# Kernel tuning notes

Hardware: AMD Instinct MI355X
Metric: run time of the kernel (lower is better)

Reference implementation:

```python
import jax, jax.numpy as jnp
import numpy as np
from jax import lax

R = 0.7          # ball-query radius
K = 32           # max neighbors per ball
STRIDE = 32      # spatial stride -> M = N // STRIDE anchors
COUT = 1024      # mlp_planes[0]


def fps(pts, M):
    """Furthest point sampling. pts: [N,3] -> int32 [M] indices (starts at 0, like CUDA FPS)."""
    N = pts.shape[0]

    def step(carry, _):
        d2, last = carry
        dist = jnp.sum((pts - pts[last]) ** 2, axis=-1)
        d2 = jnp.minimum(d2, dist)
        return (d2, jnp.argmax(d2).astype(jnp.int32)), last

    init = (jnp.full((N,), 1e10, dtype=pts.dtype), jnp.int32(0))
    _, idxs = lax.scan(step, init, None, length=M)
    return idxs


def ball_query(neigh, anchor):
    """neigh: [N,3], anchor: [M,3] -> int32 [M,K]: first K in-radius neighbor indices,
    padded with the first valid index (matching pointnet2 ball_query semantics)."""
    N = neigh.shape[0]
    d2 = jnp.sum((anchor[:, None, :] - neigh[None, :, :]) ** 2, axis=-1)  # [M,N]
    key = jnp.where(d2 < R * R, jnp.arange(N), N)  # valid points keep their position
    order = jnp.argsort(key, axis=-1)[:, :K]       # stable: first-in-order valid indices
    valid = jnp.take_along_axis(key, order, axis=-1) < N
    return jnp.where(valid, order, order[:, :1])


def setup_inputs() -> dict:
    key = jax.random.key(0)
    k1, k2 = jax.random.split(key)
    xyzs = jax.random.uniform(k1, (4, 16, 2048, 3), dtype=jnp.float32)  # points in unit cube
    w_d = jax.random.normal(k2, (COUT, 4), dtype=jnp.float32) * 0.1     # conv_d 1x1 weight
    return {"xyzs": xyzs, "w_d": w_d}


def reference(xyzs, w_d):
    B, T, N, _ = xyzs.shape
    M = N // STRIDE
    # replicate temporal padding [1,1]
    pad = jnp.concatenate([xyzs[:, :1], xyzs, xyzs[:, -1:]], axis=1)  # [B,T+2,N,3]

    anchors_src = pad[:, 1:-1].reshape(B * T, N, 3)
    aidx = jax.vmap(lambda p: fps(p, M))(anchors_src)                         # [BT,M]
    anchor = jnp.take_along_axis(anchors_src, aidx[..., None], axis=1)        # [BT,M,3]

    feat = None
    for dt in (-1, 0, 1):  # temporal kernel taps
        neigh = pad[:, 1 + dt: 1 + dt + T].reshape(B * T, N, 3)
        idx = jax.vmap(ball_query)(neigh, anchor)                             # [BT,M,K]
        grouped = jnp.take_along_axis(
            neigh, idx.reshape(B * T, M * K)[..., None], axis=1
        ).reshape(B * T, M, K, 3)
        disp = grouped - anchor[:, :, None, :]                                # xyz displacement
        d4 = jnp.concatenate(
            [disp, jnp.full((B * T, M, K, 1), float(dt), disp.dtype)], axis=-1
        )                                                                     # [BT,M,K,4]
        f = jax.nn.relu(jnp.einsum('nmkc,oc->nmko', d4, w_d))                 # 1x1 conv + ReLU
        f = jnp.max(f, axis=2)                                                # spatial max pool -> [BT,M,C]
        feat = f if feat is None else feat + f                                # temporal sum pool

    new_xyzs = anchor.reshape(B, T, M, 3)
    new_features = feat.reshape(B, T, M, COUT).transpose(0, 1, 3, 2)          # [B,T,C,M]
    return new_xyzs, new_features
```

## Files before the change

kernel.cpp:

```cpp
#include <hip/hip_runtime.h>
#include <hip/hip_fp16.h>

#define NB 4
#define NT 16
#define NN 2048
#define NM 64
#define NK 32
#define NC 1024

static __device__ inline __half2 h2max(__half2 a, __half2 b) {
    unsigned int ai = *(unsigned int*)&a, bi = *(unsigned int*)&b, di;
    asm("v_pk_max_f16 %0, %1, %2" : "=v"(di) : "v"(ai), "v"(bi));
    return *(__half2*)&di;
}
static __device__ inline unsigned long long u64max(unsigned long long a, unsigned long long b) {
    return a > b ? a : b;
}

__global__ __launch_bounds__(256) void fps_kernel(const float* __restrict__ xyzs,
                                                  float* __restrict__ out_xyz) {
    const int bt = blockIdx.x;
    const float* pts = xyzs + (size_t)bt * NN * 3;
    __shared__ float sX[NN], sY[NN], sZ[NN];
    __shared__ unsigned long long sPart[2][4];
    __shared__ float sAnchor[NM * 3];
    const int tid = threadIdx.x;
    const int lane = tid & 63, wave = tid >> 6;
    float px[8], py[8], pz[8], d2[8];
    #pragma unroll
    for (int j = 0; j < 8; ++j) {
        const int p = tid + 256 * j;
        px[j] = pts[p * 3 + 0];
        py[j] = pts[p * 3 + 1];
        pz[j] = pts[p * 3 + 2];
        sX[p] = px[j]; sY[p] = py[j]; sZ[p] = pz[j];
        d2[j] = 1e10f;
    }
    __syncthreads();
    int last = 0;
    for (int it = 0; it < NM; ++it) {
        const float lx = sX[last], ly = sY[last], lz = sZ[last];
        if (tid == 0) {
            sAnchor[it * 3 + 0] = lx; sAnchor[it * 3 + 1] = ly; sAnchor[it * 3 + 2] = lz;
        }
        float bv = -1.0f; int bj = 0;
        #pragma unroll
        for (int j = 0; j < 8; ++j) {
            const float dx = __fsub_rn(px[j], lx), dy = __fsub_rn(py[j], ly), dz = __fsub_rn(pz[j], lz);
            const float d = __fadd_rn(__fadd_rn(__fmul_rn(dx, dx), __fmul_rn(dy, dy)), __fmul_rn(dz, dz));
            d2[j] = fminf(d2[j], d);
            if (d2[j] > bv) { bv = d2[j]; bj = j; }
        }
        unsigned long long key = ((unsigned long long)__float_as_uint(bv) << 32)
                               | (unsigned)(NN - 1 - (tid + 256 * bj));
        #pragma unroll
        for (int off = 32; off > 0; off >>= 1)
            key = u64max(key, __shfl_xor(key, off, 64));
        if (lane == 0) sPart[it & 1][wave] = key;
        __syncthreads();
        key = u64max(u64max(sPart[it & 1][0], sPart[it & 1][1]),
                     u64max(sPart[it & 1][2], sPart[it & 1][3]));
        last = NN - 1 - (int)(key & 0xffffffffull);
    }
    __syncthreads();
    for (int i = tid; i < NM * 3; i += 256)
        out_xyz[bt * NM * 3 + i] = sAnchor[i];
}

__global__ __launch_bounds__(1024) void group_kernel(const float* __restrict__ xyzs,
                                                     const float* __restrict__ wd,
                                                     const float* __restrict__ anchors,
                                                     float* __restrict__ feat) {
    const int blk = blockIdx.x;
    const int bt = blk >> 2;
    const int m0 = (blk & 3) * 16;
    const int b = bt >> 4, t = bt & 15;
    __shared__ float sOut[NC * 17];
    __shared__ float sDispF[16][3][NK];
    __shared__ __align__(16) unsigned int sH[16][48];
    const int tid = threadIdx.x;
    const int lane = tid & 63, w = tid >> 6;
    const int m = m0 + w;
    const float ax = anchors[(bt * NM + m) * 3 + 0];
    const float ay = anchors[(bt * NM + m) * 3 + 1];
    const float az = anchors[(bt * NM + m) * 3 + 2];
    float acc[16];
    #pragma unroll
    for (int i = 0; i < 16; ++i) acc[i] = 0.0f;

    #pragma unroll 1
    for (int tap = 0; tap < 3; ++tap) {
        int tsrc = t + tap - 1;
        tsrc = tsrc < 0 ? 0 : (tsrc > NT - 1 ? NT - 1 : tsrc);
        const float* npts = xyzs + ((size_t)(b * NT + tsrc)) * NN * 3;
        int cnt = 0;
        for (int r = 0; r < NN / 64 && cnt < NK; ++r) {
            const int n = r * 64 + lane;
            const float dx = __fsub_rn(npts[n * 3 + 0], ax);
            const float dy = __fsub_rn(npts[n * 3 + 1], ay);
            const float dz = __fsub_rn(npts[n * 3 + 2], az);
            const float d2v = __fadd_rn(__fadd_rn(__fmul_rn(dx, dx), __fmul_rn(dy, dy)), __fmul_rn(dz, dz));
            const bool valid = d2v < 0.49f;
            const unsigned long long mask = __ballot(valid);
            const int pos = cnt + (int)__popcll(mask & ((1ull << lane) - 1ull));
            if (valid && pos < NK) {
                sDispF[w][0][pos] = dx; sDispF[w][1][pos] = dy; sDispF[w][2][pos] = dz;
            }
            cnt += (int)__popcll(mask);
        }
        if (cnt < NK) {
            float fx, fy, fz;
            if (cnt > 0) {
                fx = sDispF[w][0][0]; fy = sDispF[w][1][0]; fz = sDispF[w][2][0];
            } else {
                fx = __fsub_rn(npts[0], ax); fy = __fsub_rn(npts[1], ay); fz = __fsub_rn(npts[2], az);
            }
            if (lane >= cnt && lane < NK) {
                sDispF[w][0][lane] = fx; sDispF[w][1][lane] = fy; sDispF[w][2][lane] = fz;
            }
        }
        if (lane < 48) {
            const int c = lane >> 4, j = lane & 15;
            const float f0 = sDispF[w][c][2 * j], f1 = sDispF[w][c][2 * j + 1];
            __half2 hv = __float22half2_rn(make_float2(f0, f1));
            sH[w][c * 16 + j] = *(unsigned int*)&hv;
        }
        unsigned int hw_[48];
        #pragma unroll
        for (int i = 0; i < 12; ++i) {
            uint4 u = ((const uint4*)&sH[w][0])[i];
            hw_[4 * i + 0] = u.x; hw_[4 * i + 1] = u.y; hw_[4 * i + 2] = u.z; hw_[4 * i + 3] = u.w;
        }
        const float dtf = (float)(tap - 1);
        #pragma unroll
        for (int i = 0; i < 16; ++i) {
            const int c = lane + 64 * i;
            const float4 wv = ((const float4*)wd)[c];
            const __half2 wx = __float2half2_rn(wv.x);
            const __half2 wy = __float2half2_rn(wv.y);
            const __half2 wz = __float2half2_rn(wv.z);
            __half2 a;
            #pragma unroll
            for (int j = 0; j < 16; ++j) {
                const __half2 hx = *(const __half2*)&hw_[j];
                const __half2 hy = *(const __half2*)&hw_[16 + j];
                const __half2 hz = *(const __half2*)&hw_[32 + j];
                const __half2 s = __hfma2(wx, hx, __hfma2(wy, hy, __hmul2(wz, hz)));
                a = (j == 0) ? s : h2max(a, s);
            }
            const float mx = fmaxf(__low2float(a), __high2float(a));
            acc[i] += fmaxf(0.0f, mx + wv.w * dtf);
        }
    }
    #pragma unroll
    for (int i = 0; i < 16; ++i)
        sOut[(lane + 64 * i) * 17 + w] = acc[i];
    __syncthreads();
    {
        const int c = tid;
        float* dst = feat + ((size_t)bt * NC + c) * NM + m0;
        const float* src = &sOut[c * 17];
        #pragma unroll
        for (int r = 0; r < 4; ++r) {
            ((float4*)dst)[r] = make_float4(src[4 * r + 0], src[4 * r + 1],
                                            src[4 * r + 2], src[4 * r + 3]);
        }
    }
}

extern "C" void kernel_launch(void* const* d_in, const int* in_sizes, int n_in,
                              void* d_out, int out_size, void* d_ws, size_t ws_size,
                              hipStream_t stream) {
    const float* xyzs = (const float*)d_in[0];
    const float* wd   = (const float*)d_in[1];
    float* out_xyz = (float*)d_out;
    float* featp   = out_xyz + NB * NT * NM * 3;
    hipLaunchKernelGGL(fps_kernel, dim3(NB * NT), dim3(256), 0, stream, xyzs, out_xyz);
    hipLaunchKernelGGL(group_kernel, dim3(NB * NT * (NM / 16)), dim3(1024), 0, stream,
                       xyzs, wd, out_xyz, featp);
}
```

Measured before the change: 133.6 us.

## Split grouping into ball-query and conv kernels; reduce FPS argmax with float shuffles

The fused group kernel is split in two. A ball-query kernel runs one wave per (anchor, tap) and writes fp16 packed displacements to workspace, and a conv kernel reads them back and computes 2 channels × 4 anchors per thread, writing outputs directly without an LDS transpose. FPS now uses a blocked point layout, and its wave reduction shuffles 32-bit floats plus a ballot/ffs tie-break instead of 64-bit keys. The split raises parallelism in the serial ball-query scan and removes the 1024-thread block with large LDS, at the cost of an extra launch and a round trip through global memory.

```diff
diff --git a/kernel.cpp b/kernel.cpp
--- a/kernel.cpp
+++ b/kernel.cpp
@@ -29,7 +29,7 @@
     float px[8], py[8], pz[8], d2[8];
     #pragma unroll
     for (int j = 0; j < 8; ++j) {
-        const int p = tid + 256 * j;
+        const int p = tid * 8 + j;
         px[j] = pts[p * 3 + 0];
         py[j] = pts[p * 3 + 1];
         pz[j] = pts[p * 3 + 2];
@@ -43,23 +43,28 @@
         if (tid == 0) {
             sAnchor[it * 3 + 0] = lx; sAnchor[it * 3 + 1] = ly; sAnchor[it * 3 + 2] = lz;
         }
-        float bv = -1.0f; int bj = 0;
+        float bv = -1.0f; int bp = 0;
         #pragma unroll
         for (int j = 0; j < 8; ++j) {
             const float dx = __fsub_rn(px[j], lx), dy = __fsub_rn(py[j], ly), dz = __fsub_rn(pz[j], lz);
             const float d = __fadd_rn(__fadd_rn(__fmul_rn(dx, dx), __fmul_rn(dy, dy)), __fmul_rn(dz, dz));
             d2[j] = fminf(d2[j], d);
-            if (d2[j] > bv) { bv = d2[j]; bj = j; }
+            if (d2[j] > bv) { bv = d2[j]; bp = tid * 8 + j; }
         }
-        unsigned long long key = ((unsigned long long)__float_as_uint(bv) << 32)
-                               | (unsigned)(NN - 1 - (tid + 256 * bj));
+        float v = bv;
         #pragma unroll
         for (int off = 32; off > 0; off >>= 1)
-            key = u64max(key, __shfl_xor(key, off, 64));
-        if (lane == 0) sPart[it & 1][wave] = key;
+            v = fmaxf(v, __shfl_xor(v, off, 64));
+        const unsigned long long tied = __ballot(bv == v);
+        const int srcLane = (int)(__ffsll((long long)tied) - 1);
+        const int idxw = __shfl(bp, srcLane, 64);
+        if (lane == 0)
+            sPart[it & 1][wave] = ((unsigned long long)__float_as_uint(v) << 32)
+                                | (unsigned)(NN - 1 - idxw);
         __syncthreads();
-        key = u64max(u64max(sPart[it & 1][0], sPart[it & 1][1]),
-                     u64max(sPart[it & 1][2], sPart[it & 1][3]));
+        const unsigned long long key =
+            u64max(u64max(sPart[it & 1][0], sPart[it & 1][1]),
+                   u64max(sPart[it & 1][2], sPart[it & 1][3]));
         last = NN - 1 - (int)(key & 0xffffffffull);
     }
     __syncthreads();
@@ -67,105 +72,113 @@
         out_xyz[bt * NM * 3 + i] = sAnchor[i];
 }
 
-__global__ __launch_bounds__(1024) void group_kernel(const float* __restrict__ xyzs,
-                                                     const float* __restrict__ wd,
-                                                     const float* __restrict__ anchors,
-                                                     float* __restrict__ feat) {
-    const int blk = blockIdx.x;
-    const int bt = blk >> 2;
-    const int m0 = (blk & 3) * 16;
-    const int b = bt >> 4, t = bt & 15;
-    __shared__ float sOut[NC * 17];
-    __shared__ float sDispF[16][3][NK];
-    __shared__ __align__(16) unsigned int sH[16][48];
+__global__ __launch_bounds__(256) void bq_kernel(const float* __restrict__ xyzs,
+                                                 const float* __restrict__ anchors,
+                                                 unsigned int* __restrict__ disp) {
     const int tid = threadIdx.x;
     const int lane = tid & 63, w = tid >> 6;
-    const int m = m0 + w;
+    const int q = blockIdx.x * 4 + w;
+    const int bt = q / (NM * 3);
+    const int r = q - bt * (NM * 3);
+    const int m = r / 3, tap = r - m * 3;
+    const int b = bt >> 4, t = bt & 15;
+    __shared__ float sD[4][3][NK];
     const float ax = anchors[(bt * NM + m) * 3 + 0];
     const float ay = anchors[(bt * NM + m) * 3 + 1];
     const float az = anchors[(bt * NM + m) * 3 + 2];
-    float acc[16];
+    int tsrc = t + tap - 1;
+    tsrc = tsrc < 0 ? 0 : (tsrc > NT - 1 ? NT - 1 : tsrc);
+    const float* npts = xyzs + ((size_t)(b * NT + tsrc)) * NN * 3;
+    int cnt = 0;
+    for (int rr = 0; rr < NN / 64 && cnt < NK; ++rr) {
+        const int n = rr * 64 + lane;
+        const float dx = __fsub_rn(npts[n * 3 + 0], ax);
+        const float dy = __fsub_rn(npts[n * 3 + 1], ay);
+        const float dz = __fsub_rn(npts[n * 3 + 2], az);
+        const float d2v = __fadd_rn(__fadd_rn(__fmul_rn(dx, dx), __fmul_rn(dy, dy)), __fmul_rn(dz, dz));
+        const bool valid = d2v < 0.49f;
+        const unsigned long long mask = __ballot(valid);
+        const int pos = cnt + (int)__popcll(mask & ((1ull << lane) - 1ull));
+        if (valid && pos < NK) {
+            sD[w][0][pos] = dx; sD[w][1][pos] = dy; sD[w][2][pos] = dz;
+        }
+        cnt += (int)__popcll(mask);
+    }
+    if (cnt < NK) {
+        float fx, fy, fz;
+        if (cnt > 0) {
+            fx = sD[w][0][0]; fy = sD[w][1][0]; fz = sD[w][2][0];
+        } else {
+            fx = __fsub_rn(npts[0], ax); fy = __fsub_rn(npts[1], ay); fz = __fsub_rn(npts[2], az);
+        }
+        if (lane >= cnt && lane < NK) {
+            sD[w][0][lane] = fx; sD[w][1][lane] = fy; sD[w][2][lane] = fz;
+        }
+    }
+    if (lane < 48) {
+        const int c = lane >> 4, j = lane & 15;
+        const __half2 hv = __float22half2_rn(make_float2(sD[w][c][2 * j], sD[w][c][2 * j + 1]));
+        disp[(size_t)q * 48 + lane] = *(const unsigned int*)&hv;
+    }
+}
+
+__global__ __launch_bounds__(256) void conv_kernel(const unsigned int* __restrict__ disp,
+                                                   const float* __restrict__ wd,
+                                                   float* __restrict__ feat) {
+    const int blk = blockIdx.x;
+    const int bt = blk >> 5;
+    const int inner = blk & 31;
+    const int mh = inner >> 3, cq = inner & 7;
+    const int tid = threadIdx.x;
+    const int lane = tid & 63, w = tid >> 6;
+    const int m0 = mh * 16 + w * 4;
+    const int c0 = cq * 128 + lane;
+    const float4 wv0 = ((const float4*)wd)[c0];
+    const float4 wv1 = ((const float4*)wd)[c0 + 64];
+    const __half2 w0x = __float2half2_rn(wv0.x), w0y = __float2half2_rn(wv0.y), w0z = __float2half2_rn(wv0.z);
+    const __half2 w1x = __float2half2_rn(wv1.x), w1y = __float2half2_rn(wv1.y), w1z = __float2half2_rn(wv1.z);
+    float acc0[4], acc1[4];
     #pragma unroll
-    for (int i = 0; i < 16; ++i) acc[i] = 0.0f;
+    for (int i = 0; i < 4; ++i) { acc0[i] = 0.0f; acc1[i] = 0.0f; }
 
-    #pragma unroll 1
-    for (int tap = 0; tap < 3; ++tap) {
-        int tsrc = t + tap - 1;
-        tsrc = tsrc < 0 ? 0 : (tsrc > NT - 1 ? NT - 1 : tsrc);
-        const float* npts = xyzs + ((size_t)(b * NT + tsrc)) * NN * 3;
-        int cnt = 0;
-        for (int r = 0; r < NN / 64 && cnt < NK; ++r) {
-            const int n = r * 64 + lane;
-            const float dx = __fsub_rn(npts[n * 3 + 0], ax);
-            const float dy = __fsub_rn(npts[n * 3 + 1], ay);
-            const float dz = __fsub_rn(npts[n * 3 + 2], az);
-            const float d2v = __fadd_rn(__fadd_rn(__fmul_rn(dx, dx), __fmul_rn(dy, dy)), __fmul_rn(dz, dz));
-            const bool valid = d2v < 0.49f;
-            const unsigned long long mask = __ballot(valid);
-            const int pos = cnt + (int)__popcll(mask & ((1ull << lane) - 1ull));
-            if (valid && pos < NK) {
-                sDispF[w][0][pos] = dx; sDispF[w][1][pos] = dy; sDispF[w][2][pos] = dz;
+    #pragma unroll
+    for (int mi = 0; mi < 4; ++mi) {
+        const int m = m0 + mi;
+        #pragma unroll
+        for (int tap = 0; tap < 3; ++tap) {
+            const uint4* dp = (const uint4*)(disp + ((size_t)((bt * NM + m) * 3 + tap)) * 48);
+            unsigned int X[16], Y[16], Z[16];
+            #pragma unroll
+            for (int qq = 0; qq < 4; ++qq) {
+                uint4 u = dp[qq];
+                X[4 * qq] = u.x; X[4 * qq + 1] = u.y; X[4 * qq + 2] = u.z; X[4 * qq + 3] = u.w;
+                u = dp[4 + qq];
+                Y[4 * qq] = u.x; Y[4 * qq + 1] = u.y; Y[4 * qq + 2] = u.z; Y[4 * qq + 3] = u.w;
+                u = dp[8 + qq];
+                Z[4 * qq] = u.x; Z[4 * qq + 1] = u.y; Z[4 * qq + 2] = u.z; Z[4 * qq + 3] = u.w;
             }
-            cnt += (int)__popcll(mask);
-        }
-        if (cnt < NK) {
-            float fx, fy, fz;
-            if (cnt > 0) {
-                fx = sDispF[w][0][0]; fy = sDispF[w][1][0]; fz = sDispF[w][2][0];
-            } else {
-                fx = __fsub_rn(npts[0], ax); fy = __fsub_rn(npts[1], ay); fz = __fsub_rn(npts[2], az);
-            }
-            if (lane >= cnt && lane < NK) {
-                sDispF[w][0][lane] = fx; sDispF[w][1][lane] = fy; sDispF[w][2][lane] = fz;
-            }
-        }
-        if (lane < 48) {
-            const int c = lane >> 4, j = lane & 15;
-            const float f0 = sDispF[w][c][2 * j], f1 = sDispF[w][c][2 * j + 1];
-            __half2 hv = __float22half2_rn(make_float2(f0, f1));
-            sH[w][c * 16 + j] = *(unsigned int*)&hv;
-        }
-        unsigned int hw_[48];
-        #pragma unroll
-        for (int i = 0; i < 12; ++i) {
-            uint4 u = ((const uint4*)&sH[w][0])[i];
-            hw_[4 * i + 0] = u.x; hw_[4 * i + 1] = u.y; hw_[4 * i + 2] = u.z; hw_[4 * i + 3] = u.w;
-        }
-        const float dtf = (float)(tap - 1);
-        #pragma unroll
-        for (int i = 0; i < 16; ++i) {
-            const int c = lane + 64 * i;
-            const float4 wv = ((const float4*)wd)[c];
-            const __half2 wx = __float2half2_rn(wv.x);
-            const __half2 wy = __float2half2_rn(wv.y);
-            const __half2 wz = __float2half2_rn(wv.z);
-            __half2 a;
+            __half2 a0, a1;
             #pragma unroll
             for (int j = 0; j < 16; ++j) {
-                const __half2 hx = *(const __half2*)&hw_[j];
-                const __half2 hy = *(const __half2*)&hw_[16 + j];
-                const __half2 hz = *(const __half2*)&hw_[32 + j];
-                const __half2 s = __hfma2(wx, hx, __hfma2(wy, hy, __hmul2(wz, hz)));
-                a = (j == 0) ? s : h2max(a, s);
+                const __half2 hx = *(const __half2*)&X[j];
+                const __half2 hy = *(const __half2*)&Y[j];
+                const __half2 hz = *(const __half2*)&Z[j];
+                const __half2 s0 = __hfma2(w0x, hx, __hfma2(w0y, hy, __hmul2(w0z, hz)));
+                const __half2 s1 = __hfma2(w1x, hx, __hfma2(w1y, hy, __hmul2(w1z, hz)));
+                a0 = (j == 0) ? s0 : h2max(a0, s0);
+                a1 = (j == 0) ? s1 : h2max(a1, s1);
             }
-            const float mx = fmaxf(__low2float(a), __high2float(a));
-            acc[i] += fmaxf(0.0f, mx + wv.w * dtf);
+            const float dtf = (float)(tap - 1);
+            const float mx0 = fmaxf(__low2float(a0), __high2float(a0));
+            const float mx1 = fmaxf(__low2float(a1), __high2float(a1));
+            acc0[mi] += fmaxf(0.0f, mx0 + wv0.w * dtf);
+            acc1[mi] += fmaxf(0.0f, mx1 + wv1.w * dtf);
         }
     }
-    #pragma unroll
-    for (int i = 0; i < 16; ++i)
-        sOut[(lane + 64 * i) * 17 + w] = acc[i];
-    __syncthreads();
-    {
-        const int c = tid;
-        float* dst = feat + ((size_t)bt * NC + c) * NM + m0;
-        const float* src = &sOut[c * 17];
-        #pragma unroll
-        for (int r = 0; r < 4; ++r) {
-            ((float4*)dst)[r] = make_float4(src[4 * r + 0], src[4 * r + 1],
-                                            src[4 * r + 2], src[4 * r + 3]);
-        }
-    }
+    float* dst0 = feat + ((size_t)bt * NC + c0) * NM + m0;
+    float* dst1 = feat + ((size_t)bt * NC + c0 + 64) * NM + m0;
+    *(float4*)dst0 = make_float4(acc0[0], acc0[1], acc0[2], acc0[3]);
+    *(float4*)dst1 = make_float4(acc1[0], acc1[1], acc1[2], acc1[3]);
 }
 
 extern "C" void kernel_launch(void* const* d_in, const int* in_sizes, int n_in,
@@ -175,7 +188,10 @@
     const float* wd   = (const float*)d_in[1];
     float* out_xyz = (float*)d_out;
     float* featp   = out_xyz + NB * NT * NM * 3;
+    unsigned int* dispw = (unsigned int*)d_ws;
     hipLaunchKernelGGL(fps_kernel, dim3(NB * NT), dim3(256), 0, stream, xyzs, out_xyz);
-    hipLaunchKernelGGL(group_kernel, dim3(NB * NT * (NM / 16)), dim3(1024), 0, stream,
-                       xyzs, wd, out_xyz, featp);
+    hipLaunchKernelGGL(bq_kernel, dim3(NB * NT * NM * 3 / 4), dim3(256), 0, stream,
+                       xyzs, out_xyz, dispw);
+    hipLaunchKernelGGL(conv_kernel, dim3(2048), dim3(256), 0, stream,
+                       dispw, wd, featp);
 }
```

Result: slower. 143.2 us (+7.2%).
